# Performance work log

Hardware: AMD Instinct MI355X
Metric: run time of the kernel (lower is better)

The kernel has to match this reference:

```python
import jax, jax.numpy as jnp
import numpy as np

EPS = 1e-5
BIG = np.int32(2 ** 30)      # sentinel larger than any voxel label
L_MAX = 1024                  # fixed upper bound on number of components (jit-friendly)


def _offsets(conn):
    # 3D neighborhood offsets with at most `conn` nonzero coordinates (skimage connectivity)
    offs = []
    for dz in (-1, 0, 1):
        for dy in (-1, 0, 1):
            for dx in (-1, 0, 1):
                nz = (dz != 0) + (dy != 0) + (dx != 0)
                if 0 < nz <= conn:
                    offs.append((dz, dy, dx))
    return offs


def _ccl_26(fg):
    """Connected-component labeling, 26-connectivity (skimage.label connectivity=3).
    Iterative min-label propagation (3x3x3 min-pool) + pointer jumping.
    Returns int32 labels: 0 = background, each component gets min(flat_index)+1."""
    shape = fg.shape
    n = fg.size
    init = jnp.where(fg, jnp.arange(1, n + 1, dtype=jnp.int32).reshape(shape), 0)

    def step(labels):
        cand = jnp.where(fg, labels, BIG)
        pooled = jax.lax.reduce_window(cand, BIG, jax.lax.min, (3, 3, 3), (1, 1, 1), 'SAME')
        new = jnp.where(fg, jnp.minimum(labels, pooled), 0)
        flat = new.ravel()
        for _ in range(2):  # pointer jumping / path compression (labels are flat_index+1)
            parent = flat[jnp.maximum(flat - 1, 0)]
            flat = jnp.where(flat > 0, parent, 0)
        return flat.reshape(shape)

    def cond(c):
        old, new = c
        return jnp.any(old != new)

    def body(c):
        _, cur = c
        return cur, step(cur)

    _, final = jax.lax.while_loop(cond, body, (init, step(init)))
    return final


def _inner_boundary_18(fg):
    """skimage find_boundaries(mode='inner', connectivity=2) on 3D binary mask:
    foreground voxel with any background voxel in its 18-neighborhood
    (fg & ~erosion(fg), reflect border handling)."""
    D, H, W = fg.shape
    p = jnp.pad(fg, 1, mode='reflect')
    eroded = fg
    for dz, dy, dx in _offsets(2):
        eroded = eroded & p[1 + dz:1 + dz + D, 1 + dy:1 + dy + H, 1 + dx:1 + dx + W]
    return fg & ~eroded


def _compactness(y_pred):
    fg = y_pred > 0.5
    labels = _ccl_26(fg)                       # [D,H,W] int32
    boundary = _inner_boundary_18(fg)          # [D,H,W] bool

    # compact per-component ids (sorted unique labels, padded with BIG to stay sorted)
    uniq = jnp.unique(labels, size=L_MAX, fill_value=BIG)
    ids = jnp.searchsorted(uniq, labels).astype(jnp.int32)

    area = jax.ops.segment_sum(fg.astype(jnp.float32).ravel(), ids.ravel(), num_segments=L_MAX)
    perim = jax.ops.segment_sum(boundary.astype(jnp.float32).ravel(), ids.ravel(), num_segments=L_MAX)

    valid = (uniq > 0) & (uniq < BIG)
    # sum over z of 4*pi*area_z / (perim_3d^2 + eps) == 4*pi*total_area / (perim^2 + eps),
    # then averaged over depth D (as in the original per-label /= shape[0]).
    per_label = jnp.where(valid, 4.0 * jnp.pi * area / (perim ** 2 + EPS), 0.0)
    return jnp.sum(per_label) / y_pred.shape[0]


def setup_inputs() -> dict:
    key = jax.random.key(0)
    y_pred = jax.random.uniform(key, (64, 256, 256), dtype=jnp.float32)
    return {"y_pred": y_pred}


def reference(y_pred) -> jnp.ndarray:
    comp = _compactness(y_pred)
    return 1.0 / (comp + EPS)
```

## Files before the change

kernel.cpp:

```cpp
#include <hip/hip_runtime.h>

#define DD 64
#define HH 256
#define WW 256
#define NN (DD*HH*WW)
#define GHS 2048
#define NCOPY 16
#define PHS 131072
#define NSEG (NN/32)

#define TZ 8
#define TY 32
#define TX 32
#define TVOX (TZ*TY*TX)

#define CA 458752
#define CB 114688
#define CFACE (CA + 4*CB)

typedef float f4v __attribute__((ext_vector_type(4)));

__device__ __forceinline__ int ufind(int* P, int x){
  int p = P[x];
  while (p != x){
    int gp = P[p];
    if (gp != p) P[x] = gp;
    x = gp;
    p = P[x];
  }
  return x;
}

__device__ __forceinline__ int ufind_ro(const int* P, int x){
  int p = P[x];
  while (p != x){ x = p; p = P[x]; }
  return x;
}

__device__ __forceinline__ void uunion(int* P, int a, int b){
  while (true){
    a = ufind(P, a);
    b = ufind(P, b);
    if (a == b) return;
    if (a < b){ int t = a; a = b; b = t; }
    int old = atomicMin(&P[a], b);
    if (old == a) return;
    a = old;
  }
}

__device__ __forceinline__ int run_start(unsigned m, int x){
  unsigned zb = (~m) & ((x == 0) ? 0u : ((1u << x) - 1u));
  return (zb == 0) ? 0 : (32 - __builtin_clz(zb));
}

__device__ __forceinline__ int refl(int v, int L){ return v < 0 ? 1 : (v >= L ? L - 2 : v); }

__global__ __launch_bounds__(1024) void k_local(const float* __restrict__ in,
                                                int* __restrict__ parent,
                                                unsigned* __restrict__ fgbits,
                                                int* __restrict__ hkey,
                                                int* __restrict__ harea,
                                                int* __restrict__ hper,
                                                unsigned long long* __restrict__ ph){
  __shared__ int sl[TVOX];
  __shared__ unsigned srow[256];
  __shared__ int q[4096];
  __shared__ int qn;
  const int t = threadIdx.x;
  const int lane = t & 63;
  const int b = blockIdx.x;
  const int z0 = (b >> 6) * TZ;
  const int y0 = ((b >> 3) & 7) * TY;
  const int x0 = (b & 7) * TX;

  if (b < (NCOPY * GHS) / 1024){ int j = b * 1024 + t; hkey[j] = -1; harea[j] = 0; hper[j] = 0; }
  { int j = b * 1024 + t; if (j < PHS) ph[j] = ~0ULL; }
  if (t == 0) qn = 0;

  const int row = t >> 2;
  const int xb  = (t & 3) * 8;
  const int lz  = row >> 5, ly = row & 31;
  const int gi0 = ((z0 + lz) << 16) | ((y0 + ly) << 8) | (x0 + xb);

  const f4v* pv = (const f4v*)(in + gi0);
  f4v f0 = __builtin_nontemporal_load(pv);
  f4v f1 = __builtin_nontemporal_load(pv + 1);
  int by = (f0.x > 0.5f)        | ((f0.y > 0.5f) << 1) |
           ((f0.z > 0.5f) << 2) | ((f0.w > 0.5f) << 3) |
           ((f1.x > 0.5f) << 4) | ((f1.y > 0.5f) << 5) |
           ((f1.z > 0.5f) << 6) | ((f1.w > 0.5f) << 7);
  int v1 = by | (__shfl_xor(by, 1) << 8);
  int v2 = v1 | (__shfl_xor(v1, 2) << 16);
  if ((t & 3) == 0){
    srow[row] = (unsigned)v2;
    fgbits[((z0 + lz) << 11) | ((y0 + ly) << 3) | (x0 >> 5)] = (unsigned)v2;
  }
  __syncthreads();

  const unsigned m = srow[row];
  const unsigned starts = m & ~(m << 1);
  const unsigned sm = starts & (0xFFu << xb);

  {
    int cnt = __popc(sm);
    int pre = cnt;
    #pragma unroll
    for (int d = 1; d < 64; d <<= 1){
      int v = __shfl_up(pre, d);
      if (lane >= d) pre += v;
    }
    int tot = __shfl(pre, 63);
    int bw = 0;
    if (lane == 63) bw = atomicAdd(&qn, tot);
    bw = __shfl(bw, 63);
    int pos = bw + pre - cnt;
    unsigned w = sm;
    while (w){
      int s = __builtin_ctz(w); w &= w - 1;
      int v = (row << 5) | s;
      sl[v] = v;
      q[pos++] = v;
    }
  }
  __syncthreads();
  const int NQ = qn;

  const int rel[4][2] = {{-1,-1},{-1,0},{-1,1},{0,-1}};
  for (int it = t; it < NQ; it += 1024){
    int v = q[it];
    int vrow = v >> 5, x = v & 31;
    unsigned mr = srow[vrow];
    unsigned zs = (~mr) >> x;
    int len = zs ? __builtin_ctz(zs) : (32 - x);
    int end = x + len - 1;
    unsigned long long wmask = ((1ull << (end + 2)) - 1) &
                               ~((x == 0) ? 0ull : ((1ull << (x - 1)) - 1));
    int vlz = vrow >> 5, vly = vrow & 31;
    #pragma unroll
    for (int r = 0; r < 4; r++){
      int zz = vlz + rel[r][0], yy = vly + rel[r][1];
      if (zz < 0 || yy < 0 || yy >= TY) continue;
      int nrow = (zz << 5) | yy;
      unsigned mN = srow[nrow];
      unsigned wm = mN & (unsigned)wmask;
      while (wm){
        int bb = __builtin_ctz(wm);
        int ns = run_start(mN, bb);
        uunion(sl, v, (nrow << 5) | ns);
        unsigned t2 = (~mN) >> bb;
        int l2 = t2 ? __builtin_ctz(t2) : (32 - bb);
        unsigned long long clr = (bb + l2 >= 32) ? 0xffffffffull : ((1ull << (bb + l2)) - 1);
        wm &= ~(unsigned)clr;
      }
    }
  }
  __syncthreads();

  for (int it = t; it < NQ; it += 1024){
    int v = q[it];
    sl[v] = ufind_ro(sl, v);
  }
  __syncthreads();

  int lab[8];
  int cur = -1;
  #pragma unroll
  for (int k = 0; k < 8; k++){
    int x = xb + k;
    if (!((m >> x) & 1)){ lab[k] = -1; cur = -1; continue; }
    if (cur < 0){
      int rs = (k == 0) ? run_start(m, x) : x;
      int r = sl[(row << 5) | rs];
      cur = ((z0 + (r >> 10)) << 16) | ((y0 + ((r >> 5) & 31)) << 8) | (x0 + (r & 31));
    }
    lab[k] = cur;
  }
  *(int4*)(parent + gi0)     = make_int4(lab[0], lab[1], lab[2], lab[3]);
  *(int4*)(parent + gi0 + 4) = make_int4(lab[4], lab[5], lab[6], lab[7]);
}

__device__ __forceinline__ void phash_union(unsigned long long* H, unsigned long long key,
                                            int* parent){
  unsigned h = (unsigned)((key * 0x9E3779B97F4A7C15ull) >> 47);
  while (true){
    unsigned long long old = atomicCAS(&H[h], ~0ULL, key);
    if (old == ~0ULL){ uunion(parent, (int)(key >> 32), (int)(key & 0xffffffffu)); return; }
    if (old == key) return;
    h = (h + 1) & (PHS - 1);
  }
}

__global__ __launch_bounds__(256) void k_pairs(int* __restrict__ parent,
                                               const unsigned* __restrict__ fgbits,
                                               unsigned long long* __restrict__ ph){
  __shared__ unsigned long long pk[256];
  const int t = threadIdx.x;
  pk[t] = ~0ULL;
  __syncthreads();

  const int id = blockIdx.x * 256 + t;
  int z, y, x, ot;
  if (id < CA){ ot = 0; z = ((id >> 16) + 1) << 3; y = (id >> 8) & 255; x = id & 255; }
  else {
    int q = id - CA;
    int f = q >> 14;
    int r = q & 16383;
    int g = f / 7, mm = f % 7;
    if      (g == 0){ ot = 1; y = (mm + 1) << 5;  z = r >> 8; x = r & 255; }
    else if (g == 1){ ot = 2; y = (mm << 5) + 31; z = r >> 8; x = r & 255; }
    else if (g == 2){ ot = 3; x = (mm + 1) << 5;  z = r >> 8; y = r & 255; }
    else            { ot = 4; x = (mm << 5) + 31; z = r >> 8; y = r & 255; }
  }
  const int s = x >> 5, xl = x & 31;
  const unsigned wself = fgbits[(z << 11) | (y << 3) | s];
  if ((wself >> xl) & 1){
    const int a = parent[(z << 16) | (y << 8) | x];
    unsigned long long lastkey = ~0ULL;

    auto do_pair = [&](int zz, int yy, int xc){
      int bl = parent[(zz << 16) | (yy << 8) | xc];
      int hi = a > bl ? a : bl, lo = a > bl ? bl : a;
      unsigned long long key = ((unsigned long long)(unsigned)hi << 32) | (unsigned)lo;
      if (key == lastkey) return;
      lastkey = key;
      unsigned h = (unsigned)((key * 0x9E3779B97F4A7C15ull) >> 56);
      for (int probe = 0; probe < 256; probe++){
        unsigned long long old = atomicCAS(&pk[h], ~0ULL, key);
        if (old == ~0ULL || old == key) return;
        h = (h + 1) & 255;
      }
      phash_union(ph, key, parent);
    };

    auto do_row = [&](int zz, int yy){
      if (zz < 0 || yy < 0 || yy >= HH) return;
      unsigned mN = fgbits[(zz << 11) | (yy << 3) | s];
      if ((mN >> xl) & 1){ do_pair(zz, yy, x); return; }
      bool l = (xl > 0) ? ((mN >> (xl - 1)) & 1)
                        : (x > 0 && ((fgbits[(zz << 11) | (yy << 3) | (s - 1)] >> 31) & 1));
      bool r = (xl < 31) ? ((mN >> (xl + 1)) & 1)
                         : (x < WW - 1 && (fgbits[(zz << 11) | (yy << 3) | (s + 1)] & 1));
      if (l) do_pair(zz, yy, x - 1);
      if (r) do_pair(zz, yy, x + 1);
    };

    auto do_bit = [&](int zz, int yy, int xc){
      if (zz < 0 || yy < 0 || yy >= HH) return;
      unsigned mN = fgbits[(zz << 11) | (yy << 3) | (xc >> 5)];
      if ((mN >> (xc & 31)) & 1) do_pair(zz, yy, xc);
    };

    switch (ot){
      case 0: do_row(z-1, y-1); do_row(z-1, y); do_row(z-1, y+1); break;
      case 1: do_row(z-1, y-1); do_row(z, y-1); break;
      case 2: do_row(z-1, y+1); break;
      case 3: do_bit(z-1, y-1, x-1); do_bit(z-1, y, x-1); do_bit(z-1, y+1, x-1);
              do_bit(z,   y-1, x-1); do_bit(z,   y, x-1); break;
      case 4: do_bit(z-1, y-1, x+1); do_bit(z-1, y, x+1); do_bit(z-1, y+1, x+1);
              do_bit(z,   y-1, x+1); break;
    }
  }
  __syncthreads();
  if (pk[t] != ~0ULL) phash_union(ph, pk[t], parent);
}

__device__ __forceinline__ void ghash_add(int* hkey, int* harea, int* hper,
                                          int key, int a, int p){
  unsigned h = ((unsigned)key * 2654435761u) >> 21;
  while (true){
    int old = atomicCAS(&hkey[h], -1, key);
    if (old == -1 || old == key){
      atomicAdd(&harea[h], a);
      if (p) atomicAdd(&hper[h], p);
      return;
    }
    h = (h + 1) & (GHS - 1);
  }
}

__global__ __launch_bounds__(1024) void k_stats(const int* __restrict__ parent,
                                                const unsigned* __restrict__ fgbits,
                                                int* __restrict__ hkey,
                                                int* __restrict__ harea,
                                                int* __restrict__ hper){
  __shared__ unsigned sfg[144];
  __shared__ unsigned sbnd[32];
  __shared__ int sk[256], sa[256], sp[256];
  const int t = threadIdx.x;
  const int b = blockIdx.x;
  const int z = b >> 6;
  const int y0 = (b & 63) * 4;

  if (t < 256){ sk[t] = -1; sa[t] = 0; sp[t] = 0; }
  if (t < 144){
    int p = t / 48, q = (t / 8) % 6, s = t & 7;
    int zz = refl(z + p - 1, DD), yy = refl(y0 + q - 1, HH);
    sfg[t] = fgbits[(zz << 11) | (yy << 3) | s];
  }
  __syncthreads();

  if (t < 32){
    int ry = t >> 3, s = t & 7;
    auto W  = [&](int p, int q){ return sfg[p * 48 + q * 8 + s]; };
    auto WL = [&](int p, int q){
      unsigned w = W(p, q);
      unsigned c = (s > 0) ? ((sfg[p * 48 + q * 8 + s - 1] >> 31) & 1u) : ((w >> 1) & 1u);
      return (w << 1) | c;
    };
    auto WR = [&](int p, int q){
      unsigned w = W(p, q);
      unsigned c = (s < 7) ? ((sfg[p * 48 + q * 8 + s + 1] & 1u) << 31) : ((w & 0x40000000u) << 1);
      return (w >> 1) | c;
    };
    int qm = ry, qc = ry + 1, qp = ry + 2;
    unsigned own = W(1, qc);
    unsigned e = W(0, qm) & W(0, qp) & W(2, qm) & W(2, qp);
    e &= W(0, qc) & WL(0, qc) & WR(0, qc);
    e &= W(2, qc) & WL(2, qc) & WR(2, qc);
    e &= W(1, qm) & WL(1, qm) & WR(1, qm);
    e &= W(1, qp) & WL(1, qp) & WR(1, qp);
    e &= WL(1, qc) & WR(1, qc);
    sbnd[t] = own & ~e;
  }
  __syncthreads();

  const int i = b * 1024 + t;
  int lab = parent[i];
  int bnd = 0;
  if (lab >= 0) bnd = (sbnd[t >> 5] >> (t & 31)) & 1;

  const int lane = t & 63;
  unsigned long long fgm = __ballot(lab >= 0);
  unsigned long long bm  = __ballot(bnd != 0);
  unsigned long long act = fgm;
  while (act){
    int leader = (int)__ffsll(act) - 1;
    int llab = __shfl(lab, leader);
    unsigned long long match = __ballot(lab == llab) & fgm;
    if (lane == leader){
      int a = (int)__popcll(match);
      int p = (int)__popcll(match & bm);
      int pr = parent[llab];
      while (pr != llab){ llab = pr; pr = parent[llab]; }
      unsigned h = ((unsigned)llab * 2654435761u) >> 24;
      bool done = false;
      for (int probe = 0; probe < 256; probe++){
        int old = atomicCAS(&sk[h], -1, llab);
        if (old == -1 || old == llab){
          atomicAdd(&sa[h], a);
          if (p) atomicAdd(&sp[h], p);
          done = true; break;
        }
        h = (h + 1) & 255;
      }
      if (!done) ghash_add(hkey, harea, hper, llab, a, p);
    }
    act &= ~match;
  }
  __syncthreads();
  const int c = (b & (NCOPY - 1)) * GHS;
  if (t < 256 && sk[t] >= 0) ghash_add(hkey + c, harea + c, hper + c, sk[t], sa[t], sp[t]);
}

__global__ __launch_bounds__(1024) void k_mf(const int* __restrict__ hkey,
                                             const int* __restrict__ harea,
                                             const int* __restrict__ hper,
                                             float* __restrict__ out){
  __shared__ int mk[GHS], ma[GHS], mp[GHS];
  __shared__ float wsum[16];
  const int t = threadIdx.x;
  for (int j = t; j < GHS; j += 1024){ mk[j] = -1; ma[j] = 0; mp[j] = 0; }
  __syncthreads();
  for (int j = t; j < NCOPY * GHS; j += 1024){
    int key = hkey[j];
    if (key < 0) continue;
    int a = harea[j], p = hper[j];
    unsigned h = ((unsigned)key * 2654435761u) >> 21;
    while (true){
      int old = atomicCAS(&mk[h], -1, key);
      if (old == -1 || old == key){ atomicAdd(&ma[h], a); if (p) atomicAdd(&mp[h], p); break; }
      h = (h + 1) & (GHS - 1);
    }
  }
  __syncthreads();
  float s = 0.0f;
  for (int j = t; j < GHS; j += 1024){
    if (mk[j] >= 0){
      float a = (float)ma[j], p = (float)mp[j];
      s += 12.566370614359172f * a / (p * p + 1e-5f);
    }
  }
  #pragma unroll
  for (int d2 = 32; d2 > 0; d2 >>= 1) s += __shfl_down(s, d2);
  if ((t & 63) == 0) wsum[t >> 6] = s;
  __syncthreads();
  if (t == 0){
    float tot = 0.0f;
    #pragma unroll
    for (int k2 = 0; k2 < 16; k2++) tot += wsum[k2];
    out[0] = 1.0f / (tot / 64.0f + 1e-5f);
  }
}

extern "C" void kernel_launch(void* const* d_in, const int* in_sizes, int n_in,
                              void* d_out, int out_size, void* d_ws, size_t ws_size,
                              hipStream_t stream){
  const float* y = (const float*)d_in[0];
  char* w = (char*)d_ws;
  int* parent            = (int*)w;                    w += (size_t)NN * 4;
  unsigned long long* ph = (unsigned long long*)w;     w += (size_t)PHS * 8;
  int* hkey              = (int*)w;                    w += (size_t)NCOPY * GHS * 4;
  int* harea             = (int*)w;                    w += (size_t)NCOPY * GHS * 4;
  int* hper              = (int*)w;                    w += (size_t)NCOPY * GHS * 4;
  unsigned* fgbits       = (unsigned*)w;               w += (size_t)NSEG * 4;
  float* out = (float*)d_out;

  hipLaunchKernelGGL(k_local, dim3(512),       dim3(1024), 0, stream, y, parent, fgbits, hkey, harea, hper, ph);
  hipLaunchKernelGGL(k_pairs, dim3(CFACE/256), dim3(256),  0, stream, parent, fgbits, ph);
  hipLaunchKernelGGL(k_stats, dim3(NN/1024),   dim3(1024), 0, stream, parent, fgbits, hkey, harea, hper);
  hipLaunchKernelGGL(k_mf,    dim3(1),         dim3(1024), 0, stream, hkey, harea, hper, out);
}
```

Baseline: 168.4 us.

## Dedupe label root lookups per block, swizzle pair blocks, use plain input loads

In k_stats, each block now deduplicates the raw labels through a shared-memory hash, resolves each distinct label's root once, and then groups per wavefront by the final root instead of the provisional label. This removes repeated pointer chasing through parent done by every leader, and merging under the root can cut the number of wave-level iterations. k_pairs gets a block-index swizzle that spreads neighbouring blocks across faces, and the input load switches from nontemporal vector loads to ordinary float4 loads. The cost is extra shared-memory atomics and two more barriers per block.

```diff
diff --git a/kernel.cpp b/kernel.cpp
--- a/kernel.cpp
+++ b/kernel.cpp
@@ -17,8 +17,6 @@
 #define CA 458752
 #define CB 114688
 #define CFACE (CA + 4*CB)
-
-typedef float f4v __attribute__((ext_vector_type(4)));
 
 __device__ __forceinline__ int ufind(int* P, int x){
   int p = P[x];
@@ -83,9 +81,8 @@
   const int lz  = row >> 5, ly = row & 31;
   const int gi0 = ((z0 + lz) << 16) | ((y0 + ly) << 8) | (x0 + xb);
 
-  const f4v* pv = (const f4v*)(in + gi0);
-  f4v f0 = __builtin_nontemporal_load(pv);
-  f4v f1 = __builtin_nontemporal_load(pv + 1);
+  float4 f0 = *(const float4*)(in + gi0);
+  float4 f1 = *(const float4*)(in + gi0 + 4);
   int by = (f0.x > 0.5f)        | ((f0.y > 0.5f) << 1) |
            ((f0.z > 0.5f) << 2) | ((f0.w > 0.5f) << 3) |
            ((f1.x > 0.5f) << 4) | ((f1.y > 0.5f) << 5) |
@@ -199,7 +196,9 @@
   pk[t] = ~0ULL;
   __syncthreads();
 
-  const int id = blockIdx.x * 256 + t;
+  const int nb = (int)gridDim.x;
+  const int bsw = (blockIdx.x & 7) * (nb >> 3) + (blockIdx.x >> 3);
+  const int id = bsw * 256 + t;
   int z, y, x, ot;
   if (id < CA){ ot = 0; z = ((id >> 16) + 1) << 3; y = (id >> 8) & 255; x = id & 255; }
   else {
@@ -287,12 +286,13 @@
   __shared__ unsigned sfg[144];
   __shared__ unsigned sbnd[32];
   __shared__ int sk[256], sa[256], sp[256];
+  __shared__ int dk[256], dr[256];
   const int t = threadIdx.x;
   const int b = blockIdx.x;
   const int z = b >> 6;
   const int y0 = (b & 63) * 4;
 
-  if (t < 256){ sk[t] = -1; sa[t] = 0; sp[t] = 0; }
+  if (t < 256){ sk[t] = -1; sa[t] = 0; sp[t] = 0; dk[t] = -1; }
   if (t < 144){
     int p = t / 48, q = (t / 8) % 6, s = t & 7;
     int zz = refl(z + p - 1, DD), yy = refl(y0 + q - 1, HH);
@@ -328,21 +328,45 @@
   const int i = b * 1024 + t;
   int lab = parent[i];
   int bnd = 0;
-  if (lab >= 0) bnd = (sbnd[t >> 5] >> (t & 31)) & 1;
+  int slot = -1;
+  if (lab >= 0){
+    bnd = (sbnd[t >> 5] >> (t & 31)) & 1;
+    unsigned h = ((unsigned)lab * 2654435761u) >> 24;
+    for (int probe = 0; probe < 256; probe++){
+      int old = atomicCAS(&dk[h], -1, lab);
+      if (old == -1 || old == lab){ slot = (int)h; break; }
+      h = (h + 1) & 255;
+    }
+  }
+  __syncthreads();
+  if (t < 256 && dk[t] >= 0){
+    int l2 = dk[t];
+    int pr = parent[l2];
+    while (pr != l2){ l2 = pr; pr = parent[l2]; }
+    dr[t] = l2;
+  }
+  __syncthreads();
+  int flab = -1;
+  if (lab >= 0){
+    if (slot >= 0) flab = dr[slot];
+    else {
+      int l2 = lab, pr = parent[l2];
+      while (pr != l2){ l2 = pr; pr = parent[l2]; }
+      flab = l2;
+    }
+  }
 
   const int lane = t & 63;
-  unsigned long long fgm = __ballot(lab >= 0);
+  unsigned long long fgm = __ballot(flab >= 0);
   unsigned long long bm  = __ballot(bnd != 0);
   unsigned long long act = fgm;
   while (act){
     int leader = (int)__ffsll(act) - 1;
-    int llab = __shfl(lab, leader);
-    unsigned long long match = __ballot(lab == llab) & fgm;
+    int llab = __shfl(flab, leader);
+    unsigned long long match = __ballot(flab == llab) & fgm;
     if (lane == leader){
       int a = (int)__popcll(match);
       int p = (int)__popcll(match & bm);
-      int pr = parent[llab];
-      while (pr != llab){ llab = pr; pr = parent[llab]; }
       unsigned h = ((unsigned)llab * 2654435761u) >> 24;
       bool done = false;
       for (int probe = 0; probe < 256; probe++){
```

Measured after the change: 164.1 us. 1.03x faster.
